# Kernel tuning notes

Hardware: AMD Instinct MI355X
Metric: run time of the kernel (lower is better)

The kernel has to match this reference:

```python
import jax, jax.numpy as jnp
import numpy as np

DECAY = 0.1
EPS = 1e-5


def setup_inputs() -> dict:
    key = jax.random.key(0)
    k1, k2, k3, k4 = jax.random.split(key, 4)
    N, K, D = 262144, 1024, 64
    x = jax.random.normal(k1, (N, D), dtype=jnp.float32)
    embed = jax.random.normal(k2, (K, D), dtype=jnp.float32) * 0.01
    cluster_size = jax.random.uniform(k3, (K,), dtype=jnp.float32)
    embed_avg = jax.random.normal(k4, (K, D), dtype=jnp.float32) * 0.01
    return {"x": x, "embed": embed, "cluster_size": cluster_size, "embed_avg": embed_avg}


def reference(x, embed, cluster_size, embed_avg):
    # x: [N, D] flattened latents; embed: [K, D] codebook
    N, D = x.shape
    K = embed.shape[0]

    # Squared Euclidean distance (same argmin as torch.cdist p=2).
    x2 = jnp.sum(x * x, axis=-1, keepdims=True)            # [N, 1]
    e2 = jnp.sum(embed * embed, axis=-1)                   # [K]
    dist = x2 - 2.0 * jnp.einsum('nd,kd->nk', x, embed) + e2[None, :]  # [N, K]
    embed_ind = jnp.argmin(dist, axis=-1)                  # [N] int

    # Quantize: gather nearest codes.
    quantize = embed[embed_ind]                            # [N, D]

    # --- EMA codebook update (no-grad in the original) ---
    xs = jax.lax.stop_gradient(x)
    bins = jax.ops.segment_sum(jnp.ones((N,), dtype=x.dtype), embed_ind,
                               num_segments=K)             # [K] bincount
    embed_sum = jax.ops.segment_sum(xs, embed_ind, num_segments=K)  # [K, D] scatter-add

    cluster_size_new = cluster_size * DECAY + bins * (1.0 - DECAY)
    embed_avg_new = embed_avg * DECAY + embed_sum * (1.0 - DECAY)

    # Laplace smoothing then normalize to get the updated codebook.
    n = jnp.sum(cluster_size_new)
    cs_smoothed = (cluster_size_new + EPS) / (n + K * EPS) * n
    embed_normalized = embed_avg_new / cs_smoothed[:, None]  # [K, D]

    return quantize, embed_ind, cluster_size_new, embed_avg_new, embed_normalized
```

## Files before the change

### kernel.cpp

```cpp
#include <hip/hip_runtime.h>
#include <hip/hip_bf16.h>


#define NROWS 262144
#define KCODES 1024
#define DDIM 64
#define CAPL 4

typedef __attribute__((ext_vector_type(8))) short short8;
typedef __attribute__((ext_vector_type(4))) float f32x4;

__device__ __forceinline__ unsigned short f2bf(float f) {
    unsigned u = __float_as_uint(f);
    unsigned r = u + 0x7fffu + ((u >> 16) & 1u);
    return (unsigned short)(r >> 16);
}

__global__ __launch_bounds__(256) void vq_prep(
    const float* __restrict__ embed, unsigned short* __restrict__ eb,
    float* __restrict__ e2f, float* __restrict__ enmax2)
{
    const int k = blockIdx.x * 256 + threadIdx.x;
    const float* er = embed + (size_t)k * DDIM;
    float s = 0.f;
    #pragma unroll
    for (int d = 0; d < DDIM; ++d) { float v = er[d]; s = fmaf(v, v, s); }
    e2f[k] = s;
    #pragma unroll
    for (int d = 0; d < DDIM; ++d) eb[(size_t)k * DDIM + d] = f2bf(er[d]);
    atomicMax((int*)enmax2, __float_as_int(s));
}

__global__ __launch_bounds__(512) void vq_phaseA(
    const float* __restrict__ x, const unsigned short* __restrict__ eb,
    const float* __restrict__ e2f, const float* __restrict__ enmax2,
    float* __restrict__ out_ind, int* __restrict__ candg, int* __restrict__ cntg,
    int* __restrict__ wl, int* __restrict__ gcount,
    int* __restrict__ wl2, int* __restrict__ gcount2, int* __restrict__ bins_i)
{
    __shared__ __align__(16) unsigned short ebs[16384];
    __shared__ float e2L[256];
    __shared__ float norm2L[256];
    __shared__ int   cntL[256];
    __shared__ int   candL[256][CAPL];
    __shared__ int   mcount, mbase, mcount2, mbase2;

    const int t    = threadIdx.x;
    const int lane = t & 63;
    const int wid  = t >> 6;
    const int col  = lane & 15;
    const int q    = lane >> 4;
    const int rowb = blockIdx.x * 256;
    const int r0   = wid * 32;

    short8 a0[2], a1[2];
    {
        const float* xr = x + (size_t)(rowb + r0 + col) * DDIM;
        float s = 0.f;
        #pragma unroll
        for (int m = 0; m < 2; ++m) {
            const float4 u = *reinterpret_cast<const float4*>(xr + m * 32 + 8 * q);
            const float4 v = *reinterpret_cast<const float4*>(xr + m * 32 + 8 * q + 4);
            short8 f;
            f[0] = (short)f2bf(u.x); f[1] = (short)f2bf(u.y);
            f[2] = (short)f2bf(u.z); f[3] = (short)f2bf(u.w);
            f[4] = (short)f2bf(v.x); f[5] = (short)f2bf(v.y);
            f[6] = (short)f2bf(v.z); f[7] = (short)f2bf(v.w);
            a0[m] = f;
            s = fmaf(u.x, u.x, s); s = fmaf(u.y, u.y, s);
            s = fmaf(u.z, u.z, s); s = fmaf(u.w, u.w, s);
            s = fmaf(v.x, v.x, s); s = fmaf(v.y, v.y, s);
            s = fmaf(v.z, v.z, s); s = fmaf(v.w, v.w, s);
        }
        s += __shfl_xor(s, 16); s += __shfl_xor(s, 32);
        if (lane < 16) norm2L[r0 + lane] = s;
    }
    {
        const float* xr = x + (size_t)(rowb + r0 + 16 + col) * DDIM;
        float s = 0.f;
        #pragma unroll
        for (int m = 0; m < 2; ++m) {
            const float4 u = *reinterpret_cast<const float4*>(xr + m * 32 + 8 * q);
            const float4 v = *reinterpret_cast<const float4*>(xr + m * 32 + 8 * q + 4);
            short8 f;
            f[0] = (short)f2bf(u.x); f[1] = (short)f2bf(u.y);
            f[2] = (short)f2bf(u.z); f[3] = (short)f2bf(u.w);
            f[4] = (short)f2bf(v.x); f[5] = (short)f2bf(v.y);
            f[6] = (short)f2bf(v.z); f[7] = (short)f2bf(v.w);
            a1[m] = f;
            s = fmaf(u.x, u.x, s); s = fmaf(u.y, u.y, s);
            s = fmaf(u.z, u.z, s); s = fmaf(u.w, u.w, s);
            s = fmaf(v.x, v.x, s); s = fmaf(v.y, v.y, s);
            s = fmaf(v.z, v.z, s); s = fmaf(v.w, v.w, s);
        }
        s += __shfl_xor(s, 16); s += __shfl_xor(s, 32);
        if (lane < 16) norm2L[r0 + 16 + lane] = s;
    }

    if (t < 256) cntL[t] = 0;
    if (t == 0) { mcount = 0; mcount2 = 0; }
    const float en2 = *enmax2;

    const int off0 = col * 128 + ((q       ^ (col & 7)) << 4);
    const int off1 = col * 128 + (((4 + q) ^ (col & 7)) << 4);

    f32x4 best0, best1;
    #pragma unroll
    for (int r = 0; r < 4; ++r) { best0[r] = -3.4e38f; best1[r] = -3.4e38f; }

#define STAGE16(P)                                                            \
    _Pragma("unroll")                                                         \
    for (int it = 0; it < 4; ++it) {                                          \
        const int f16 = t + it * 512;                                         \
        const int cp  = f16 >> 3, slot = f16 & 7;                             \
        const short8 v = *reinterpret_cast<const short8*>(                    \
            eb + (size_t)(P) * 16384 + (size_t)f16 * 8);                      \
        *reinterpret_cast<short8*>((char*)ebs + (cp >> 5) * 4096 +            \
            (cp & 31) * 128 + ((slot ^ (cp & 7)) << 4)) = v;                  \
    }                                                                         \
    if (t < 256) e2L[t] = -0.5f * e2f[(P) * 256 + t];

#define CHUNKS(P, KIND)                                                       \
    _Pragma("unroll")                                                         \
    for (int ch = 0; ch < 16; ++ch) {                                         \
        const short8 b0 = *reinterpret_cast<const short8*>(                   \
            (char*)ebs + ch * 2048 + off0);                                   \
        const short8 b1 = *reinterpret_cast<const short8*>(                   \
            (char*)ebs + ch * 2048 + off1);                                   \
        const float e2n = e2L[ch * 16 + col];                                 \
        f32x4 acc0, acc1;                                                     \
        acc0[0] = e2n; acc0[1] = e2n; acc0[2] = e2n; acc0[3] = e2n;           \
        acc1 = acc0;                                                          \
        acc0 = __builtin_amdgcn_mfma_f32_16x16x32_bf16(a0[0], b0, acc0, 0, 0, 0); \
        acc1 = __builtin_amdgcn_mfma_f32_16x16x32_bf16(a1[0], b0, acc1, 0, 0, 0); \
        acc0 = __builtin_amdgcn_mfma_f32_16x16x32_bf16(a0[1], b1, acc0, 0, 0, 0); \
        acc1 = __builtin_amdgcn_mfma_f32_16x16x32_bf16(a1[1], b1, acc1, 0, 0, 0); \
        if (KIND == 0) {                                                      \
            _Pragma("unroll")                                                 \
            for (int r = 0; r < 4; ++r) {                                     \
                best0[r] = fmaxf(best0[r], acc0[r]);                          \
                best1[r] = fmaxf(best1[r], acc1[r]);                          \
            }                                                                 \
        } else {                                                              \
            _Pragma("unroll")                                                 \
            for (int r = 0; r < 4; ++r) {                                     \
                if (acc0[r] >= best0[r]) {                                    \
                    const int rl = r0 + q * 4 + r;                            \
                    const int idx = atomicAdd(&cntL[rl], 1);                  \
                    if (idx < CAPL) candL[rl][idx] = (P) * 256 + ch * 16 + col; \
                }                                                             \
                if (acc1[r] >= best1[r]) {                                    \
                    const int rl = r0 + 16 + q * 4 + r;                       \
                    const int idx = atomicAdd(&cntL[rl], 1);                  \
                    if (idx < CAPL) candL[rl][idx] = (P) * 256 + ch * 16 + col; \
                }                                                             \
            }                                                                 \
        }                                                                     \
    }

    for (int p = 0; p < 4; ++p) {
        __syncthreads();
        STAGE16(p)
        __syncthreads();
        CHUNKS(p, 0)
    }

    #pragma unroll
    for (int r = 0; r < 4; ++r) {
        float v0 = best0[r], v1 = best1[r];
        v0 = fmaxf(v0, __shfl_xor(v0, 1));  v1 = fmaxf(v1, __shfl_xor(v1, 1));
        v0 = fmaxf(v0, __shfl_xor(v0, 2));  v1 = fmaxf(v1, __shfl_xor(v1, 2));
        v0 = fmaxf(v0, __shfl_xor(v0, 4));  v1 = fmaxf(v1, __shfl_xor(v1, 4));
        v0 = fmaxf(v0, __shfl_xor(v0, 8));  v1 = fmaxf(v1, __shfl_xor(v1, 8));
        const int lr = q * 4 + r;
        const float m0 = 0.0078125f * sqrtf(norm2L[r0 + lr] * en2) + 5e-5f;
        const float m1 = 0.0078125f * sqrtf(norm2L[r0 + 16 + lr] * en2) + 5e-5f;
        best0[r] = v0 - m0;
        best1[r] = v1 - m1;
    }

    CHUNKS(3, 1)
    for (int p = 0; p < 3; ++p) {
        __syncthreads();
        STAGE16(p)
        __syncthreads();
        CHUNKS(p, 1)
    }
    __syncthreads();

    int my = -1, my2 = -1, c = 0;
    if (t < 256) {
        c = cntL[t];
        if (c == 1) {
            const int code = candL[t][0];
            out_ind[rowb + t] = (float)code;
            atomicAdd(bins_i + code, 1);
        }
        else if (c <= CAPL)   my  = atomicAdd(&mcount, 1);
        else                  my2 = atomicAdd(&mcount2, 1);
    }
    __syncthreads();
    if (t == 0) { mbase = atomicAdd(gcount, mcount); mbase2 = atomicAdd(gcount2, mcount2); }
    __syncthreads();
    if (my >= 0) {
        const int row = rowb + t;
        wl[mbase + my] = row;
        cntg[row] = c;
        #pragma unroll
        for (int j = 0; j < CAPL; ++j)
            if (j < c) candg[row * CAPL + j] = candL[t][j];
    }
    if (my2 >= 0) wl2[mbase2 + my2] = rowb + t;
#undef STAGE16
#undef CHUNKS
}

__global__ __launch_bounds__(256) void vq_rerank1(
    const float* __restrict__ x, const float* __restrict__ embed,
    const float* __restrict__ e2f, const int* __restrict__ wl,
    const int* __restrict__ gcount, const int* __restrict__ cntg,
    const int* __restrict__ candg, float* __restrict__ out_ind,
    int* __restrict__ bins_i)
{
    const int n = *gcount;
    for (int i = blockIdx.x * 256 + threadIdx.x; i < n; i += gridDim.x * 256) {
        const int row = wl[i];
        float xv[DDIM];
        {
            const float4* xp = reinterpret_cast<const float4*>(x + (size_t)row * DDIM);
            float4 xq[16];
            #pragma unroll
            for (int qq = 0; qq < 16; ++qq) xq[qq] = xp[qq];
            #pragma unroll
            for (int qq = 0; qq < 16; ++qq) {
                xv[qq*4+0] = xq[qq].x; xv[qq*4+1] = xq[qq].y;
                xv[qq*4+2] = xq[qq].z; xv[qq*4+3] = xq[qq].w;
            }
        }
        float x2 = 0.f;
        #pragma unroll
        for (int d = 0; d < DDIM; ++d) x2 = fmaf(xv[d], xv[d], x2);

        const int c = cntg[row];
        float bv = 3.4e38f; int bk = 0x7fffffff;
        for (int ci = 0; ci < c; ++ci) {
            const int k = candg[row * CAPL + ci];
            const float4* ep = reinterpret_cast<const float4*>(embed + (size_t)k * DDIM);
            float dot = 0.f;
            #pragma unroll
            for (int qq = 0; qq < 16; ++qq) {
                const float4 e4 = ep[qq];
                dot = fmaf(xv[qq*4+0], e4.x, dot);
                dot = fmaf(xv[qq*4+1], e4.y, dot);
                dot = fmaf(xv[qq*4+2], e4.z, dot);
                dot = fmaf(xv[qq*4+3], e4.w, dot);
            }
            const float dist = (x2 - 2.0f * dot) + e2f[k];
            if (dist < bv || (dist == bv && k < bk)) { bv = dist; bk = k; }
        }
        out_ind[row] = (float)bk;
        atomicAdd(bins_i + bk, 1);
    }
}

__global__ __launch_bounds__(256) void vq_rerank2(
    const float* __restrict__ x, const float* __restrict__ embed,
    const float* __restrict__ e2f, const int* __restrict__ wl2,
    const int* __restrict__ gcount2, float* __restrict__ out_ind,
    int* __restrict__ bins_i)
{
    const int t    = threadIdx.x;
    const int lane = t & 63;
    const int gw   = (blockIdx.x * 256 + t) >> 6;
    const int nw   = (gridDim.x * 256) >> 6;
    const int n    = *gcount2;

    for (int e = gw; e < n; e += nw) {
        const int row = wl2[e];
        float xv[DDIM];
        {
            const float4* xp = reinterpret_cast<const float4*>(x + (size_t)row * DDIM);
            #pragma unroll
            for (int qq = 0; qq < 16; ++qq) {
                const float4 v = xp[qq];
                xv[qq*4+0] = v.x; xv[qq*4+1] = v.y; xv[qq*4+2] = v.z; xv[qq*4+3] = v.w;
            }
        }
        float x2 = 0.f;
        #pragma unroll
        for (int d = 0; d < DDIM; ++d) x2 = fmaf(xv[d], xv[d], x2);

        float bv = 3.4e38f; int bk = 0x7fffffff;
        for (int k = lane; k < KCODES; k += 64) {
            const float* er = embed + (size_t)k * DDIM;
            float dot = 0.f;
            #pragma unroll
            for (int d = 0; d < DDIM; ++d) dot = fmaf(xv[d], er[d], dot);
            const float dist = (x2 - 2.0f * dot) + e2f[k];
            if (dist < bv) { bv = dist; bk = k; }
        }
        #pragma unroll
        for (int s = 1; s < 64; s <<= 1) {
            const float ov = __shfl_xor(bv, s);
            const int   ok = __shfl_xor(bk, s);
            if (ov < bv || (ov == bv && ok < bk)) { bv = ov; bk = ok; }
        }
        if (lane == 0) { out_ind[row] = (float)bk; atomicAdd(bins_i + bk, 1); }
    }
}

__global__ __launch_bounds__(1024) void vq_prefix(
    const int* __restrict__ bins_i, int* __restrict__ offs, int* __restrict__ cursor)
{
    __shared__ int s[KCODES];
    const int t = threadIdx.x;
    const int b = bins_i[t];
    s[t] = b;
    __syncthreads();
    for (int d = 1; d < KCODES; d <<= 1) {
        const int v = (t >= d) ? s[t - d] : 0;
        __syncthreads();
        s[t] += v;
        __syncthreads();
    }
    const int excl = s[t] - b;
    offs[t] = excl;
    cursor[t] = excl;
}

__global__ __launch_bounds__(256) void vq_scatter(
    const float* __restrict__ out_ind, int* __restrict__ cursor, int* __restrict__ sorted)
{
    const int row  = blockIdx.x * 256 + threadIdx.x;
    const int code = (int)out_ind[row];
    const int pos  = atomicAdd(cursor + code, 1);
    sorted[pos] = (code << 20) | row;
}

__global__ __launch_bounds__(256) void vq_reduce(
    const float* __restrict__ x, const int* __restrict__ sorted,
    float* __restrict__ esum)
{
    const int t = threadIdx.x, lane = t & 63, w = t >> 6;
    const int p0 = (blockIdx.x * 4 + w) * 64;

    int cur = sorted[p0] >> 20;
    float acc = 0.f;
    #pragma unroll 4
    for (int i = 0; i < 64; i += 4) {
        const int4 e4 = *reinterpret_cast<const int4*>(sorted + p0 + i);
        const float v0 = x[(size_t)(e4.x & 0xFFFFF) * DDIM + lane];
        const float v1 = x[(size_t)(e4.y & 0xFFFFF) * DDIM + lane];
        const float v2 = x[(size_t)(e4.z & 0xFFFFF) * DDIM + lane];
        const float v3 = x[(size_t)(e4.w & 0xFFFFF) * DDIM + lane];
        const int c0 = e4.x >> 20, c1 = e4.y >> 20, c2 = e4.z >> 20, c3 = e4.w >> 20;
        if (c0 != cur) { unsafeAtomicAdd(esum + cur * DDIM + lane, acc); acc = 0.f; cur = c0; }
        acc += v0;
        if (c1 != cur) { unsafeAtomicAdd(esum + cur * DDIM + lane, acc); acc = 0.f; cur = c1; }
        acc += v1;
        if (c2 != cur) { unsafeAtomicAdd(esum + cur * DDIM + lane, acc); acc = 0.f; cur = c2; }
        acc += v2;
        if (c3 != cur) { unsafeAtomicAdd(esum + cur * DDIM + lane, acc); acc = 0.f; cur = c3; }
        acc += v3;
    }
    unsafeAtomicAdd(esum + cur * DDIM + lane, acc);
}

__global__ __launch_bounds__(1024) void vq_finalize(
    const float* __restrict__ cluster_size, const float* __restrict__ embed_avg,
    const int* __restrict__ bins_i, float* __restrict__ out_cs,
    float* __restrict__ out_eavg, float* __restrict__ out_enorm)
{
    __shared__ float red[KCODES];
    __shared__ float css[KCODES];
    const int t = threadIdx.x;

    const float csn = cluster_size[t] * 0.1f + (float)bins_i[t] * 0.9f;
    red[t] = csn;
    __syncthreads();
    for (int s = 512; s > 0; s >>= 1) {
        if (t < s) red[t] += red[t + s];
        __syncthreads();
    }
    const float n = red[0];
    out_cs[t] = csn;
    css[t] = (csn + 1e-5f) / (n + (float)(KCODES * 1e-5)) * n;
    __syncthreads();

    #pragma unroll
    for (int i = 0; i < 16; ++i) {
        const int f4 = t + i * 1024;
        const int k  = f4 >> 4;
        const float4 ea = reinterpret_cast<const float4*>(embed_avg)[f4];
        const float4 su = reinterpret_cast<const float4*>(out_eavg)[f4];
        const float  cc = css[k];
        float4 ean, en;
        ean.x = ea.x * 0.1f + su.x * 0.9f; en.x = ean.x / cc;
        ean.y = ea.y * 0.1f + su.y * 0.9f; en.y = ean.y / cc;
        ean.z = ea.z * 0.1f + su.z * 0.9f; en.z = ean.z / cc;
        ean.w = ea.w * 0.1f + su.w * 0.9f; en.w = ean.w / cc;
        reinterpret_cast<float4*>(out_eavg)[f4]  = ean;
        reinterpret_cast<float4*>(out_enorm)[f4] = en;
    }
}

__global__ __launch_bounds__(256) void vq_quant(
    const float* __restrict__ out_ind, const float* __restrict__ embed,
    float* __restrict__ out_q)
{
    __shared__ int inds[256];
    const int t = threadIdx.x;
    const int row0 = blockIdx.x * 256;
    inds[t] = (int)out_ind[row0 + t];
    __syncthreads();
    #pragma unroll
    for (int i = 0; i < 16; ++i) {
        const int f = t + i * 256;
        const int r = f >> 4, dq = f & 15;
        const int code = inds[r];
        const float4 ev = *reinterpret_cast<const float4*>(
            embed + (size_t)code * DDIM + dq * 4);
        *reinterpret_cast<float4*>(out_q + (size_t)(row0 + r) * DDIM + dq * 4) = ev;
    }
}

extern "C" void kernel_launch(void* const* d_in, const int* in_sizes, int n_in,
                              void* d_out, int out_size, void* d_ws, size_t ws_size,
                              hipStream_t stream)
{
    const float* x            = (const float*)d_in[0];
    const float* embed        = (const float*)d_in[1];
    const float* cluster_size = (const float*)d_in[2];
    const float* embed_avg    = (const float*)d_in[3];

    float* out      = (float*)d_out;
    float* out_q    = out;
    float* out_ind  = out_q + (size_t)NROWS * DDIM;
    float* out_cs   = out_ind + NROWS;
    float* out_eavg = out_cs + KCODES;
    float* out_en   = out_eavg + (size_t)KCODES * DDIM;

    unsigned short* eb = (unsigned short*)out_en;
    float* e2f = out_en + 32768;

    int* S      = (int*)out_q;
    int* candg  = S;
    int* cntg   = S + 1048576;
    int* wl     = S + 1310720;
    int* wl2    = S + 1572864;
    int* sorted = S + 1835008;
    int* bins_i = S + 2097152;
    int* gcount = bins_i + KCODES;
    int* gcount2= gcount + 1;
    float* enmax2 = (float*)(gcount2 + 1);
    int* offs   = gcount2 + 2;
    int* cursor = offs + KCODES;

    hipMemsetAsync(bins_i, 0, (KCODES + 3) * sizeof(int), stream);
    hipMemsetAsync(out_eavg, 0, (size_t)KCODES * DDIM * sizeof(float), stream);

    vq_prep    <<<KCODES / 256, 256, 0, stream>>>(embed, eb, e2f, enmax2);
    vq_phaseA  <<<NROWS / 256, 512, 0, stream>>>(x, eb, e2f, enmax2, out_ind,
                                                 candg, cntg, wl, gcount,
                                                 wl2, gcount2, bins_i);
    vq_rerank1 <<<512, 256, 0, stream>>>(x, embed, e2f, wl, gcount, cntg, candg,
                                         out_ind, bins_i);
    vq_rerank2 <<<128, 256, 0, stream>>>(x, embed, e2f, wl2, gcount2, out_ind, bins_i);
    vq_prefix  <<<1, 1024, 0, stream>>>(bins_i, offs, cursor);
    vq_scatter <<<NROWS / 256, 256, 0, stream>>>(out_ind, cursor, sorted);
    vq_reduce  <<<NROWS / 256, 256, 0, stream>>>(x, sorted, out_eavg);
    vq_finalize<<<1, 1024, 0, stream>>>(cluster_size, embed_avg, bins_i,
                                        out_cs, out_eavg, out_en);
    vq_quant   <<<NROWS / 256, 256, 0, stream>>>(out_ind, embed, out_q);
}
```

Baseline: 334.6 us.

## Double-buffer codebook staging with async global-to-LDS loads and pre-swizzled layout

The prep kernel now writes the bf16 codebook already in the swizzled LDS layout, so phaseA can copy it with direct global_load_lds instructions instead of register round-trips. PhaseA double-buffers the codebook quarters so loading the next quarter overlaps the MFMA work on the current one, halving barriers, and loads all e2 values once up front. The two rerank kernels are merged into one launch, and an unused offsets array is dropped. LDS use doubles (about 64KB+), which may limit occupancy.

```diff
diff --git a/kernel.cpp b/kernel.cpp
--- a/kernel.cpp
+++ b/kernel.cpp
@@ -26,8 +26,15 @@
     #pragma unroll
     for (int d = 0; d < DDIM; ++d) { float v = er[d]; s = fmaf(v, v, s); }
     e2f[k] = s;
-    #pragma unroll
-    for (int d = 0; d < DDIM; ++d) eb[(size_t)k * DDIM + d] = f2bf(er[d]);
+    unsigned char* base = (unsigned char*)eb + (k >> 8) * 32768 +
+                          ((k >> 5) & 7) * 4096 + (k & 31) * 128;
+    #pragma unroll
+    for (int sl = 0; sl < 8; ++sl) {
+        short8 f;
+        #pragma unroll
+        for (int j = 0; j < 8; ++j) f[j] = (short)f2bf(er[sl * 8 + j]);
+        *reinterpret_cast<short8*>(base + ((sl ^ (k & 7)) << 4)) = f;
+    }
     atomicMax((int*)enmax2, __float_as_int(s));
 }
 
@@ -38,8 +45,9 @@
     int* __restrict__ wl, int* __restrict__ gcount,
     int* __restrict__ wl2, int* __restrict__ gcount2, int* __restrict__ bins_i)
 {
-    __shared__ __align__(16) unsigned short ebs[16384];
-    __shared__ float e2L[256];
+    __shared__ __align__(16) unsigned short ebs0[16384];
+    __shared__ __align__(16) unsigned short ebs1[16384];
+    __shared__ float e2L[KCODES];
     __shared__ float norm2L[256];
     __shared__ int   cntL[256];
     __shared__ int   candL[256][CAPL];
@@ -52,6 +60,21 @@
     const int q    = lane >> 4;
     const int rowb = blockIdx.x * 256;
     const int r0   = wid * 32;
+
+#define STAGEQ(BUF, P)                                                        \
+    {                                                                         \
+        const unsigned char* gsrc = (const unsigned char*)eb +                \
+            (size_t)(P) * 32768 + t * 16;                                     \
+        unsigned char* ldst = (unsigned char*)(BUF) + t * 16;                 \
+        _Pragma("unroll")                                                     \
+        for (int it = 0; it < 4; ++it)                                        \
+            __builtin_amdgcn_global_load_lds(                                 \
+                (const __attribute__((address_space(1))) void*)(gsrc + it * 8192), \
+                (__attribute__((address_space(3))) void*)(ldst + it * 8192),  \
+                16, 0, 0);                                                    \
+    }
+
+    STAGEQ(ebs0, 0)
 
     short8 a0[2], a1[2];
     {
@@ -97,6 +120,8 @@
         if (lane < 16) norm2L[r0 + 16 + lane] = s;
     }
 
+    e2L[t]       = -0.5f * e2f[t];
+    e2L[512 + t] = -0.5f * e2f[512 + t];
     if (t < 256) cntL[t] = 0;
     if (t == 0) { mcount = 0; mcount2 = 0; }
     const float en2 = *enmax2;
@@ -108,26 +133,14 @@
     #pragma unroll
     for (int r = 0; r < 4; ++r) { best0[r] = -3.4e38f; best1[r] = -3.4e38f; }
 
-#define STAGE16(P)                                                            \
-    _Pragma("unroll")                                                         \
-    for (int it = 0; it < 4; ++it) {                                          \
-        const int f16 = t + it * 512;                                         \
-        const int cp  = f16 >> 3, slot = f16 & 7;                             \
-        const short8 v = *reinterpret_cast<const short8*>(                    \
-            eb + (size_t)(P) * 16384 + (size_t)f16 * 8);                      \
-        *reinterpret_cast<short8*>((char*)ebs + (cp >> 5) * 4096 +            \
-            (cp & 31) * 128 + ((slot ^ (cp & 7)) << 4)) = v;                  \
-    }                                                                         \
-    if (t < 256) e2L[t] = -0.5f * e2f[(P) * 256 + t];
-
-#define CHUNKS(P, KIND)                                                       \
+#define CHUNKS(BUF, P, KIND)                                                  \
     _Pragma("unroll")                                                         \
     for (int ch = 0; ch < 16; ++ch) {                                         \
         const short8 b0 = *reinterpret_cast<const short8*>(                   \
-            (char*)ebs + ch * 2048 + off0);                                   \
+            (char*)(BUF) + ch * 2048 + off0);                                 \
         const short8 b1 = *reinterpret_cast<const short8*>(                   \
-            (char*)ebs + ch * 2048 + off1);                                   \
-        const float e2n = e2L[ch * 16 + col];                                 \
+            (char*)(BUF) + ch * 2048 + off1);                                 \
+        const float e2n = e2L[(P) * 256 + ch * 16 + col];                     \
         f32x4 acc0, acc1;                                                     \
         acc0[0] = e2n; acc0[1] = e2n; acc0[2] = e2n; acc0[3] = e2n;           \
         acc1 = acc0;                                                          \
@@ -158,12 +171,11 @@
         }                                                                     \
     }
 
-    for (int p = 0; p < 4; ++p) {
-        __syncthreads();
-        STAGE16(p)
-        __syncthreads();
-        CHUNKS(p, 0)
-    }
+    __syncthreads();
+    STAGEQ(ebs1, 1)  CHUNKS(ebs0, 0, 0)  __syncthreads();
+    STAGEQ(ebs0, 2)  CHUNKS(ebs1, 1, 0)  __syncthreads();
+    STAGEQ(ebs1, 3)  CHUNKS(ebs0, 2, 0)  __syncthreads();
+    CHUNKS(ebs1, 3, 0)
 
     #pragma unroll
     for (int r = 0; r < 4; ++r) {
@@ -179,13 +191,10 @@
         best1[r] = v1 - m1;
     }
 
-    CHUNKS(3, 1)
-    for (int p = 0; p < 3; ++p) {
-        __syncthreads();
-        STAGE16(p)
-        __syncthreads();
-        CHUNKS(p, 1)
-    }
+    STAGEQ(ebs0, 0)  CHUNKS(ebs1, 3, 1)  __syncthreads();
+    STAGEQ(ebs1, 1)  CHUNKS(ebs0, 0, 1)  __syncthreads();
+    STAGEQ(ebs0, 2)  CHUNKS(ebs1, 1, 1)  __syncthreads();
+    CHUNKS(ebs0, 2, 1)
     __syncthreads();
 
     int my = -1, my2 = -1, c = 0;
@@ -211,19 +220,21 @@
             if (j < c) candg[row * CAPL + j] = candL[t][j];
     }
     if (my2 >= 0) wl2[mbase2 + my2] = rowb + t;
-#undef STAGE16
+#undef STAGEQ
 #undef CHUNKS
 }
 
-__global__ __launch_bounds__(256) void vq_rerank1(
+__global__ __launch_bounds__(256) void vq_rerank(
     const float* __restrict__ x, const float* __restrict__ embed,
     const float* __restrict__ e2f, const int* __restrict__ wl,
     const int* __restrict__ gcount, const int* __restrict__ cntg,
-    const int* __restrict__ candg, float* __restrict__ out_ind,
+    const int* __restrict__ candg, const int* __restrict__ wl2,
+    const int* __restrict__ gcount2, float* __restrict__ out_ind,
     int* __restrict__ bins_i)
 {
+    const int t = threadIdx.x;
     const int n = *gcount;
-    for (int i = blockIdx.x * 256 + threadIdx.x; i < n; i += gridDim.x * 256) {
+    for (int i = blockIdx.x * 256 + t; i < n; i += gridDim.x * 256) {
         const int row = wl[i];
         float xv[DDIM];
         {
@@ -261,21 +272,12 @@
         out_ind[row] = (float)bk;
         atomicAdd(bins_i + bk, 1);
     }
-}
-
-__global__ __launch_bounds__(256) void vq_rerank2(
-    const float* __restrict__ x, const float* __restrict__ embed,
-    const float* __restrict__ e2f, const int* __restrict__ wl2,
-    const int* __restrict__ gcount2, float* __restrict__ out_ind,
-    int* __restrict__ bins_i)
-{
-    const int t    = threadIdx.x;
+
     const int lane = t & 63;
     const int gw   = (blockIdx.x * 256 + t) >> 6;
     const int nw   = (gridDim.x * 256) >> 6;
-    const int n    = *gcount2;
-
-    for (int e = gw; e < n; e += nw) {
+    const int n2   = *gcount2;
+    for (int e = gw; e < n2; e += nw) {
         const int row = wl2[e];
         float xv[DDIM];
         {
@@ -310,7 +312,7 @@
 }
 
 __global__ __launch_bounds__(1024) void vq_prefix(
-    const int* __restrict__ bins_i, int* __restrict__ offs, int* __restrict__ cursor)
+    const int* __restrict__ bins_i, int* __restrict__ cursor)
 {
     __shared__ int s[KCODES];
     const int t = threadIdx.x;
@@ -323,9 +325,7 @@
         s[t] += v;
         __syncthreads();
     }
-    const int excl = s[t] - b;
-    offs[t] = excl;
-    cursor[t] = excl;
+    cursor[t] = s[t] - b;
 }
 
 __global__ __launch_bounds__(256) void vq_scatter(
@@ -453,8 +453,7 @@
     int* gcount = bins_i + KCODES;
     int* gcount2= gcount + 1;
     float* enmax2 = (float*)(gcount2 + 1);
-    int* offs   = gcount2 + 2;
-    int* cursor = offs + KCODES;
+    int* cursor = gcount2 + 2;
 
     hipMemsetAsync(bins_i, 0, (KCODES + 3) * sizeof(int), stream);
     hipMemsetAsync(out_eavg, 0, (size_t)KCODES * DDIM * sizeof(float), stream);
@@ -463,10 +462,9 @@
     vq_phaseA  <<<NROWS / 256, 512, 0, stream>>>(x, eb, e2f, enmax2, out_ind,
                                                  candg, cntg, wl, gcount,
                                                  wl2, gcount2, bins_i);
-    vq_rerank1 <<<512, 256, 0, stream>>>(x, embed, e2f, wl, gcount, cntg, candg,
-                                         out_ind, bins_i);
-    vq_rerank2 <<<128, 256, 0, stream>>>(x, embed, e2f, wl2, gcount2, out_ind, bins_i);
-    vq_prefix  <<<1, 1024, 0, stream>>>(bins_i, offs, cursor);
+    vq_rerank  <<<512, 256, 0, stream>>>(x, embed, e2f, wl, gcount, cntg, candg,
+                                         wl2, gcount2, out_ind, bins_i);
+    vq_prefix  <<<1, 1024, 0, stream>>>(bins_i, cursor);
     vq_scatter <<<NROWS / 256, 256, 0, stream>>>(out_ind, cursor, sorted);
     vq_reduce  <<<NROWS / 256, 256, 0, stream>>>(x, sorted, out_eavg);
     vq_finalize<<<1, 1024, 0, stream>>>(cluster_size, embed_avg, bins_i,
```

Result: faster. 304.0 us (-9.1%).
